# Kernel tuning notes

Hardware: AMD Instinct MI355X
Metric: run time of the kernel (lower is better)

## Reference

```python
import jax, jax.numpy as jnp
import numpy as np

COMMITMENT_WEIGHT = 1.0


def setup_inputs() -> dict:
    key = jax.random.key(0)
    k1, k2 = jax.random.split(key)
    N, D, K, H = 32768, 512, 8192, 1
    x = jax.random.normal(k1, (N, D), dtype=jnp.float32)
    embed = jax.random.normal(k2, (H, K, D), dtype=jnp.float32)
    return {"x": x, "embed": embed}


def reference(x, embed):
    # x: [N, D] -> add codebook dim (needs_codebook_dim path): [H, N, D]
    xf = x.astype(jnp.float32)[None, ...]                      # [1, N, D]
    x_sq = jnp.sum(xf * xf, axis=-1, keepdims=True)            # [H, N, 1]
    e_sq = jnp.sum(embed * embed, axis=-1)                     # [H, K]
    dots = jnp.einsum('hnd,hkd->hnk', xf, embed)               # [H, N, K]
    dist = x_sq - 2.0 * dots + e_sq[:, None, :]                # [H, N, K]
    embed_ind = jnp.argmin(dist, axis=-1)                      # [H, N]
    # codebook lookup (equivalent to one_hot @ embed)
    quantize = jax.vmap(lambda e, i: e[i])(embed, embed_ind)   # [H, N, D]
    # commitment loss (quantize detached vs encoder output)
    commit_loss = jnp.mean((jax.lax.stop_gradient(quantize) - xf) ** 2) * COMMITMENT_WEIGHT
    # straight-through estimator
    quantize = xf + jax.lax.stop_gradient(quantize - xf)
    # drop the added codebook dim
    return quantize[0], embed_ind[0], commit_loss
```

## Files before the change

### kernel.cpp

```cpp
#include <hip/hip_runtime.h>

#define N_ROWS 32768
#define DIM 512
#define K_CODES 8192

#define TMI 128
#define TNI 256
#define BKE 64
#define NKTI (DIM / BKE)
#define QSCALE 32.0f
#define SCL (2.0f / (QSCALE * QSCALE))
#define EPS_I8 5.0f
#define QMARG 2.2f
#define SLOTS 64

#define BN 64
#define BK 256
#define BD 32

typedef __attribute__((ext_vector_type(8))) short bf16x8;
typedef __attribute__((ext_vector_type(4))) float f32x4;
typedef __attribute__((ext_vector_type(4))) int i32x4;

#define AS1 __attribute__((address_space(1)))
#define AS3 __attribute__((address_space(3)))

__device__ inline unsigned int ord_f32(float f) {
    unsigned int u = __float_as_uint(f);
    return (u & 0x80000000u) ? ~u : (u | 0x80000000u);
}
__device__ inline float unord_f32(unsigned int u) {
    unsigned int b = (u & 0x80000000u) ? (u & 0x7fffffffu) : ~u;
    return __uint_as_float(b);
}
__device__ inline int q8(float f) {
    int t = __float2int_rn(f * QSCALE);
    t = t < -127 ? -127 : t;
    t = t > 127 ? 127 : t;
    return t & 255;
}
__device__ inline int pack4(float4 v) {
    return q8(v.x) | (q8(v.y) << 8) | (q8(v.z) << 16) | (q8(v.w) << 24);
}

__global__ __launch_bounds__(256) void esq_kernel(const float* __restrict__ embed,
                                                  float* __restrict__ e_sq) {
    int code = blockIdx.x * 4 + (threadIdx.x >> 6);
    int lane = threadIdx.x & 63;
    const float4* row = (const float4*)(embed + (size_t)code * DIM);
    float s = 0.f;
#pragma unroll
    for (int i = 0; i < 2; ++i) {
        float4 v = row[lane + i * 64];
        s += v.x * v.x + v.y * v.y + v.z * v.z + v.w * v.w;
    }
#pragma unroll
    for (int off = 32; off > 0; off >>= 1) s += __shfl_down(s, off);
    if (lane == 0) e_sq[code] = s;
}

__global__ __launch_bounds__(256) void cvt_embed_i8_kernel(const float* __restrict__ embed,
                                                           signed char* __restrict__ eq,
                                                           float* __restrict__ e_sq) {
    int code = blockIdx.x * 4 + (threadIdx.x >> 6);
    int lane = threadIdx.x & 63;
    const float4* row = (const float4*)(embed + (size_t)code * DIM);
    float4 v0 = row[lane * 2], v1 = row[lane * 2 + 1];
    float s = v0.x * v0.x + v0.y * v0.y + v0.z * v0.z + v0.w * v0.w
            + v1.x * v1.x + v1.y * v1.y + v1.z * v1.z + v1.w * v1.w;
    int2 o;
    o.x = pack4(v0);
    o.y = pack4(v1);
    *(int2*)(eq + (size_t)code * DIM + lane * 8) = o;
#pragma unroll
    for (int off = 32; off > 0; off >>= 1) s += __shfl_down(s, off);
    if (lane == 0) e_sq[code] = s;
}

__global__ __launch_bounds__(256) void cvt_x_i8_kernel(const float* __restrict__ in,
                                                       signed char* __restrict__ out, int n16) {
    int i = blockIdx.x * 256 + threadIdx.x;
    if (i >= n16) return;
    const float4* p = (const float4*)in + (size_t)i * 4;
    float4 v0 = p[0], v1 = p[1], v2 = p[2], v3 = p[3];
    int4 o;
    o.x = pack4(v0); o.y = pack4(v1); o.z = pack4(v2); o.w = pack4(v3);
    ((int4*)out)[i] = o;
}

__global__ __launch_bounds__(512, 4) void passA_i8_kernel(const signed char* __restrict__ xq,
                                                          const signed char* __restrict__ eq,
                                                          const float* __restrict__ e_sq,
                                                          unsigned int* __restrict__ cand_count,
                                                          unsigned int* __restrict__ cands) {
    __shared__ __align__(16) signed char As[3][TMI * BKE];
    __shared__ __align__(16) signed char Bs[3][TNI * BKE];

    const int tid = threadIdx.x;
    const int lane = tid & 63;
    const int wv = tid >> 6;
    const int wm = wv >> 2, wn = wv & 3;
    const int l15 = lane & 15, l4 = lane >> 4;
    const int slot = l4 ^ ((l15 >> 1) & 3);

    const int bid = blockIdx.x;
    const int xcd = bid & 7, idx = bid >> 3;
    const int bx = xcd * 4 + (idx >> 8);
    const int by = idx & 255;
    const int row0 = by * TMI;
    const int col0 = bx * TNI;

    const int cA = tid, cB0 = tid, cB1 = tid + 512;
    const int qA = ((cA & 3) ^ ((cA >> 3) & 3)) * 16;
    const int qB0 = ((cB0 & 3) ^ ((cB0 >> 3) & 3)) * 16;
    const int qB1 = ((cB1 & 3) ^ ((cB1 >> 3) & 3)) * 16;
    const signed char* xr = xq + (size_t)(row0 + (cA >> 2)) * DIM + qA;
    const signed char* er0 = eq + (size_t)(col0 + (cB0 >> 2)) * DIM + qB0;
    const signed char* er1 = eq + (size_t)(col0 + (cB1 >> 2)) * DIM + qB1;

    i32x4 acc[4][4];
#pragma unroll
    for (int m = 0; m < 4; ++m)
#pragma unroll
        for (int n = 0; n < 4; ++n) acc[m][n] = i32x4{0, 0, 0, 0};

#define STAGE(sl, kt)                                                                               \
    do {                                                                                            \
        __builtin_amdgcn_global_load_lds((const AS1 void*)(xr + (kt)),                              \
                                         (AS3 void*)&As[sl][cA * 16], 16, 0, 0);                    \
        __builtin_amdgcn_global_load_lds((const AS1 void*)(er0 + (kt)),                             \
                                         (AS3 void*)&Bs[sl][cB0 * 16], 16, 0, 0);                   \
        __builtin_amdgcn_global_load_lds((const AS1 void*)(er1 + (kt)),                             \
                                         (AS3 void*)&Bs[sl][cB1 * 16], 16, 0, 0);                   \
    } while (0)

    STAGE(0, 0);
    STAGE(1, BKE);
#pragma unroll
    for (int t = 0; t < NKTI; ++t) {
        if (t + 1 < NKTI) {
            asm volatile("s_waitcnt vmcnt(3)" ::: "memory");
        } else {
            asm volatile("s_waitcnt vmcnt(0)" ::: "memory");
        }
        __builtin_amdgcn_s_barrier();
        if (t + 2 < NKTI) STAGE((t + 2) % 3, (t + 2) * BKE);
        const int buf = t % 3;
        i32x4 bfr[4], af[4];
#pragma unroll
        for (int n = 0; n < 4; ++n)
            bfr[n] = *(const i32x4*)&Bs[buf][(wn * 64 + n * 16 + l15) * BKE + slot * 16];
#pragma unroll
        for (int m = 0; m < 4; ++m)
            af[m] = *(const i32x4*)&As[buf][(wm * 64 + m * 16 + l15) * BKE + slot * 16];
        __builtin_amdgcn_s_setprio(1);
#pragma unroll
        for (int m = 0; m < 4; ++m)
#pragma unroll
            for (int n = 0; n < 4; ++n)
                acc[m][n] = __builtin_amdgcn_mfma_i32_16x16x64_i8(af[m], bfr[n], acc[m][n], 0, 0, 0);
        __builtin_amdgcn_s_setprio(0);
    }
#undef STAGE

    unsigned int* row_min = (unsigned int*)&As[0][0];

    float esr[4];
#pragma unroll
    for (int n = 0; n < 4; ++n) esr[n] = e_sq[col0 + wn * 64 + n * 16 + l15];

    __syncthreads();
    if (tid < TMI) row_min[tid] = 0xFFFFFFFFu;
    __syncthreads();
#pragma unroll
    for (int m = 0; m < 4; ++m) {
        float rv[4];
#pragma unroll
        for (int r = 0; r < 4; ++r) rv[r] = 3.4e38f;
#pragma unroll
        for (int n = 0; n < 4; ++n)
#pragma unroll
            for (int r = 0; r < 4; ++r) {
                float s = fmaf(-SCL, (float)acc[m][n][r], esr[n]);
                acc[m][n][r] = __float_as_int(s);
                rv[r] = fminf(rv[r], s);
            }
#pragma unroll
        for (int d = 1; d < 16; d <<= 1)
#pragma unroll
            for (int r = 0; r < 4; ++r) rv[r] = fminf(rv[r], __shfl_xor(rv[r], d));
        if (l15 == 0) {
#pragma unroll
            for (int r = 0; r < 4; ++r)
                atomicMin(&row_min[wm * 64 + m * 16 + l4 * 4 + r], ord_f32(rv[r]));
        }
    }
    __syncthreads();
#pragma unroll
    for (int m = 0; m < 4; ++m)
#pragma unroll
        for (int r = 0; r < 4; ++r) {
            const int lrow = wm * 64 + m * 16 + l4 * 4 + r;
            const float th = unord_f32(row_min[lrow]) + EPS_I8;
            const int grow = row0 + lrow;
#pragma unroll
            for (int n = 0; n < 4; ++n) {
                float sv = __int_as_float(acc[m][n][r]);
                if (sv <= th) {
                    unsigned int s = atomicAdd(&cand_count[grow], 1u);
                    if (s < SLOTS) {
                        unsigned int code = (unsigned)(col0 + wn * 64 + n * 16 + l15);
                        cands[(size_t)grow * SLOTS + s] = (ord_f32(sv) & 0xFFFFE000u) | code;
                    }
                }
            }
        }
}

__global__ __launch_bounds__(256) void passA_fp32_kernel(const float* __restrict__ x,
                                                         const float* __restrict__ embed,
                                                         const float* __restrict__ e_sq,
                                                         unsigned int* __restrict__ cand_count,
                                                         unsigned int* __restrict__ cands,
                                                         int slots) {
    __shared__ float xs[BD][BN];
    __shared__ float es[BD][BK];
    __shared__ float bbest[BN];
    __shared__ unsigned long long smin[BN][33];

    const int tid = threadIdx.x;
    const int tx = tid & 31, ty = tid >> 5;
    const int kb = blockIdx.x * BK;
    const int nb = blockIdx.y * BN;

    float acc[8][8];
#pragma unroll
    for (int i = 0; i < 8; ++i)
#pragma unroll
        for (int j = 0; j < 8; ++j) acc[i][j] = 0.f;

    for (int dt = 0; dt < DIM; dt += BD) {
        {
            int row = tid >> 2, seg = tid & 3;
            const float* xp = x + (size_t)(nb + row) * DIM + dt + seg * 4;
            float4 v0 = *(const float4*)(xp);
            float4 v1 = *(const float4*)(xp + 16);
            xs[seg * 4 + 0][row] = v0.x;  xs[seg * 4 + 1][row] = v0.y;
            xs[seg * 4 + 2][row] = v0.z;  xs[seg * 4 + 3][row] = v0.w;
            xs[seg * 4 + 16][row] = v1.x; xs[seg * 4 + 17][row] = v1.y;
            xs[seg * 4 + 18][row] = v1.z; xs[seg * 4 + 19][row] = v1.w;
        }
        {
            const float* ep = embed + (size_t)(kb + tid) * DIM + dt;
            float4 v[8];
#pragma unroll
            for (int i = 0; i < 8; ++i) v[i] = *(const float4*)(ep + i * 4);
#pragma unroll
            for (int i = 0; i < 8; ++i) {
                es[i * 4 + 0][tid] = v[i].x; es[i * 4 + 1][tid] = v[i].y;
                es[i * 4 + 2][tid] = v[i].z; es[i * 4 + 3][tid] = v[i].w;
            }
        }
        __syncthreads();
#pragma unroll
        for (int d = 0; d < BD; ++d) {
            float a[8], b[8];
            float4 a0 = *(const float4*)&xs[d][ty * 8];
            float4 a1 = *(const float4*)&xs[d][ty * 8 + 4];
            a[0] = a0.x; a[1] = a0.y; a[2] = a0.z; a[3] = a0.w;
            a[4] = a1.x; a[5] = a1.y; a[6] = a1.z; a[7] = a1.w;
#pragma unroll
            for (int j = 0; j < 8; ++j) b[j] = es[d][tx + j * 32];
#pragma unroll
            for (int i = 0; i < 8; ++i)
#pragma unroll
                for (int j = 0; j < 8; ++j) acc[i][j] = fmaf(a[i], b[j], acc[i][j]);
        }
        __syncthreads();
    }

    float esr[8];
#pragma unroll
    for (int j = 0; j < 8; ++j) esr[j] = e_sq[kb + tx + j * 32];
#pragma unroll
    for (int i = 0; i < 8; ++i) {
        float best = 3.4e38f;
#pragma unroll
        for (int j = 0; j < 8; ++j) {
            acc[i][j] = fmaf(-2.f, acc[i][j], esr[j]);
            if (acc[i][j] < best) best = acc[i][j];
        }
        smin[ty * 8 + i][tx] = ((unsigned long long)ord_f32(best) << 32);
    }
    __syncthreads();
    if (tid < BN) {
        unsigned long long m = smin[tid][0];
#pragma unroll 4
        for (int c = 1; c < 32; ++c) {
            unsigned long long v = smin[tid][c];
            if (v < m) m = v;
        }
        bbest[tid] = unord_f32((unsigned int)(m >> 32));
    }
    __syncthreads();
#pragma unroll
    for (int i = 0; i < 8; ++i) {
        int row = ty * 8 + i;
        float thr = bbest[row] + 1.5f;
#pragma unroll
        for (int j = 0; j < 8; ++j) {
            if (acc[i][j] <= thr) {
                unsigned int slot = atomicAdd(&cand_count[nb + row], 1u);
                if (slot < (unsigned)slots)
                    cands[(size_t)(nb + row) * slots + slot] =
                        (ord_f32(acc[i][j]) & 0xFFFFE000u) | (unsigned)(kb + tx + j * 32);
            }
        }
    }
}

__global__ __launch_bounds__(256) void refine_kernel(const float* __restrict__ x,
                                                     const float* __restrict__ embed,
                                                     const unsigned int* __restrict__ cand_count,
                                                     const unsigned int* __restrict__ cands,
                                                     int slots,
                                                     float* __restrict__ out_q,
                                                     float* __restrict__ out_ind,
                                                     double* __restrict__ partials) {
    __shared__ double s_score[64];
    __shared__ unsigned int s_idx[64];
    __shared__ unsigned int s_minkey;
    __shared__ int s_ns;
    __shared__ int s_best;
    __shared__ float s_ls[4];

    const int row = blockIdx.x;
    const int tid = threadIdx.x;
    const int wave = tid >> 6, lane = tid & 63;
    const unsigned int craw = cand_count[row];
    const float4* xp = (const float4*)(x + (size_t)row * DIM);

    if (craw <= (unsigned)slots) {
        int c = (int)craw;
        if (c < 1) c = 1;
        if (tid < 64) {
            unsigned int k = (tid < c) ? cands[(size_t)row * slots + tid] : 0xFFFFFFFFu;
#pragma unroll
            for (int d = 1; d < 64; d <<= 1) {
                unsigned int o = (unsigned int)__shfl_xor((int)k, d);
                if (o < k) k = o;
            }
            if (tid == 0) { s_minkey = k; s_ns = 0; }
        }
        __syncthreads();
        const float th = unord_f32(s_minkey & 0xFFFFE000u) + EPS_I8 + QMARG;
        if (tid < c) {
            unsigned int k = cands[(size_t)row * slots + tid];
            if (unord_f32(k & 0xFFFFE000u) <= th) {
                int sl = atomicAdd(&s_ns, 1);
                s_idx[sl] = k & 0x1FFFu;
            }
        }
        __syncthreads();
        const int ns = s_ns;
        for (int ci = wave; ci < ns; ci += 4) {
            unsigned int k = s_idx[ci];
            const float4* ep = (const float4*)(embed + (size_t)k * DIM);
            double s = 0.0;
#pragma unroll
            for (int i = 0; i < 2; ++i) {
                float4 ev = ep[lane + i * 64];
                float4 xv = xp[lane + i * 64];
                s += (double)ev.x * ((double)ev.x - 2.0 * (double)xv.x);
                s += (double)ev.y * ((double)ev.y - 2.0 * (double)xv.y);
                s += (double)ev.z * ((double)ev.z - 2.0 * (double)xv.z);
                s += (double)ev.w * ((double)ev.w - 2.0 * (double)xv.w);
            }
#pragma unroll
            for (int off = 32; off > 0; off >>= 1) s += __shfl_down(s, off);
            if (lane == 0) s_score[ci] = s;
        }
        __syncthreads();
        if (tid == 0) {
            double best = s_score[0];
            unsigned int bidx = s_idx[0];
            for (int ci = 1; ci < ns; ++ci) {
                double sv = s_score[ci];
                unsigned int k = s_idx[ci];
                if (sv < best || (sv == best && k < bidx)) { best = sv; bidx = k; }
            }
            s_best = (int)bidx;
            out_ind[row] = (float)bidx;
        }
    } else {
        double wbest = 1e300;
        int wbidx = 0;
        for (int k = wave; k < K_CODES; k += 4) {
            const float4* ep = (const float4*)(embed + (size_t)k * DIM);
            double s = 0.0;
#pragma unroll
            for (int i = 0; i < 2; ++i) {
                float4 ev = ep[lane + i * 64];
                float4 xv = xp[lane + i * 64];
                s += (double)ev.x * ((double)ev.x - 2.0 * (double)xv.x);
                s += (double)ev.y * ((double)ev.y - 2.0 * (double)xv.y);
                s += (double)ev.z * ((double)ev.z - 2.0 * (double)xv.z);
                s += (double)ev.w * ((double)ev.w - 2.0 * (double)xv.w);
            }
#pragma unroll
            for (int off = 32; off > 0; off >>= 1) s += __shfl_down(s, off);
            if (lane == 0 && s < wbest) { wbest = s; wbidx = k; }
        }
        if (lane == 0) { s_score[wave] = wbest; s_idx[wave] = (unsigned)wbidx; }
        __syncthreads();
        if (tid == 0) {
            double best = s_score[0];
            unsigned int bidx = s_idx[0];
            for (int w = 1; w < 4; ++w) {
                if (s_score[w] < best || (s_score[w] == best && s_idx[w] < bidx)) {
                    best = s_score[w]; bidx = s_idx[w];
                }
            }
            s_best = (int)bidx;
            out_ind[row] = (float)bidx;
        }
    }
    __syncthreads();
    const int k = s_best;
    const float2* x2 = (const float2*)(x + (size_t)row * DIM);
    const float2* e2 = (const float2*)(embed + (size_t)k * DIM);
    float2* o2 = (float2*)(out_q + (size_t)row * DIM);
    float2 xv = x2[tid], ev = e2[tid];
    float2 o;
    o.x = xv.x + (ev.x - xv.x);
    o.y = xv.y + (ev.y - xv.y);
    o2[tid] = o;
    float dx = ev.x - xv.x, dy = ev.y - xv.y;
    float ls = dx * dx + dy * dy;
#pragma unroll
    for (int off = 32; off > 0; off >>= 1) ls += __shfl_down(ls, off);
    if (lane == 0) s_ls[wave] = ls;
    __syncthreads();
    if (tid == 0) partials[row] = (double)(s_ls[0] + s_ls[1] + s_ls[2] + s_ls[3]);
}

__global__ __launch_bounds__(1024) void finalize_kernel(const double* __restrict__ partials,
                                                        float* __restrict__ out_loss) {
    __shared__ double sm[1024];
    double s = 0.0;
    for (int i = threadIdx.x; i < N_ROWS; i += 1024) s += partials[i];
    sm[threadIdx.x] = s;
    __syncthreads();
    for (int off = 512; off > 0; off >>= 1) {
        if (threadIdx.x < off) sm[threadIdx.x] += sm[threadIdx.x + off];
        __syncthreads();
    }
    if (threadIdx.x == 0) *out_loss = (float)(sm[0] / ((double)N_ROWS * (double)DIM));
}

extern "C" void kernel_launch(void* const* d_in, const int* in_sizes, int n_in,
                              void* d_out, int out_size, void* d_ws, size_t ws_size,
                              hipStream_t stream) {
    const float* x = (const float*)d_in[0];
    const float* embed = (const float*)d_in[1];
    float* out = (float*)d_out;
    float* out_q = out;
    float* out_ind = out + (size_t)N_ROWS * DIM;
    float* out_loss = out_ind + N_ROWS;

    char* ws = (char*)d_ws;
    float* e_sq = (float*)(ws + 16);
    unsigned int* counts = (unsigned int*)(ws + 16 + 32768);
    double* partials = (double*)(ws + 16 + 32768 + 131072);
    char* dyn = ws + 16 + 32768 + 131072 + 262144;
    size_t fixed = (size_t)16 + 32768 + 131072 + 262144;
    size_t dyn_avail = ws_size > fixed ? ws_size - fixed : 0;

    const size_t xq_b = (size_t)N_ROWS * DIM;
    const size_t eq_b = (size_t)K_CODES * DIM;
    const size_t need_i8 = xq_b + eq_b + (size_t)N_ROWS * SLOTS * 4;

    hipMemsetAsync(counts, 0, (size_t)N_ROWS * 4, stream);

    if (dyn_avail >= need_i8) {
        signed char* xq = (signed char*)dyn;
        signed char* eq = (signed char*)(dyn + xq_b);
        unsigned int* cands = (unsigned int*)(dyn + xq_b + eq_b);
        cvt_embed_i8_kernel<<<K_CODES / 4, 256, 0, stream>>>(embed, eq, e_sq);
        cvt_x_i8_kernel<<<(N_ROWS * DIM / 16 + 255) / 256, 256, 0, stream>>>(x, xq, N_ROWS * DIM / 16);
        passA_i8_kernel<<<(K_CODES / TNI) * (N_ROWS / TMI), 512, 0, stream>>>(xq, eq, e_sq, counts, cands);
        refine_kernel<<<N_ROWS, 256, 0, stream>>>(x, embed, counts, cands, SLOTS, out_q, out_ind, partials);
    } else {
        esq_kernel<<<K_CODES / 4, 256, 0, stream>>>(embed, e_sq);
        unsigned int* cands = (unsigned int*)dyn;
        int slots = 40;
        size_t avail = dyn_avail / ((size_t)N_ROWS * 4);
        if (avail < (size_t)slots) slots = (int)avail;
        if (slots < 2) slots = 2;
        passA_fp32_kernel<<<dim3(K_CODES / BK, N_ROWS / BN), 256, 0, stream>>>(x, embed, e_sq, counts, cands, slots);
        refine_kernel<<<N_ROWS, 256, 0, stream>>>(x, embed, counts, cands, slots, out_q, out_ind, partials);
    }
    finalize_kernel<<<1, 1024, 0, stream>>>(partials, out_loss);
}
```

Baseline: 476.3 us.

## Enlarge int8 distance GEMM tile to 256x256 with double-buffered LDS

Doubles the row tile of the int8 distance pass so each wave computes 128x64 outputs, raising arithmetic intensity and halving reloads of codebook tiles. LDS staging changes from a three-deep to a two-deep ring, with an explicit barrier after each k-step to protect the buffer being overwritten. The trade-off is much higher accumulator register pressure under the same launch bounds, fewer blocks in the grid, and less latency hiding from the shallower pipeline.

```diff
diff --git a/kernel.cpp b/kernel.cpp
--- a/kernel.cpp
+++ b/kernel.cpp
@@ -4,7 +4,7 @@
 #define DIM 512
 #define K_CODES 8192
 
-#define TMI 128
+#define TMI 256
 #define TNI 256
 #define BKE 64
 #define NKTI (DIM / BKE)
@@ -18,7 +18,6 @@
 #define BK 256
 #define BD 32
 
-typedef __attribute__((ext_vector_type(8))) short bf16x8;
 typedef __attribute__((ext_vector_type(4))) float f32x4;
 typedef __attribute__((ext_vector_type(4))) int i32x4;
 
@@ -93,8 +92,8 @@
                                                           const float* __restrict__ e_sq,
                                                           unsigned int* __restrict__ cand_count,
                                                           unsigned int* __restrict__ cands) {
-    __shared__ __align__(16) signed char As[3][TMI * BKE];
-    __shared__ __align__(16) signed char Bs[3][TNI * BKE];
+    __shared__ __align__(16) signed char As[2][TMI * BKE];
+    __shared__ __align__(16) signed char Bs[2][TNI * BKE];
 
     const int tid = threadIdx.x;
     const int lane = tid & 63;
@@ -105,61 +104,66 @@
 
     const int bid = blockIdx.x;
     const int xcd = bid & 7, idx = bid >> 3;
-    const int bx = xcd * 4 + (idx >> 8);
-    const int by = idx & 255;
+    const int bx = xcd * 4 + (idx >> 7);
+    const int by = idx & 127;
     const int row0 = by * TMI;
     const int col0 = bx * TNI;
 
-    const int cA = tid, cB0 = tid, cB1 = tid + 512;
-    const int qA = ((cA & 3) ^ ((cA >> 3) & 3)) * 16;
-    const int qB0 = ((cB0 & 3) ^ ((cB0 >> 3) & 3)) * 16;
-    const int qB1 = ((cB1 & 3) ^ ((cB1 >> 3) & 3)) * 16;
-    const signed char* xr = xq + (size_t)(row0 + (cA >> 2)) * DIM + qA;
-    const signed char* er0 = eq + (size_t)(col0 + (cB0 >> 2)) * DIM + qB0;
-    const signed char* er1 = eq + (size_t)(col0 + (cB1 >> 2)) * DIM + qB1;
-
-    i32x4 acc[4][4];
-#pragma unroll
-    for (int m = 0; m < 4; ++m)
+    const int c0 = tid, c1 = tid + 512;
+    const int q0 = ((c0 & 3) ^ ((c0 >> 3) & 3)) * 16;
+    const int q1 = ((c1 & 3) ^ ((c1 >> 3) & 3)) * 16;
+    const signed char* xr0 = xq + (size_t)(row0 + (c0 >> 2)) * DIM + q0;
+    const signed char* xr1 = xq + (size_t)(row0 + (c1 >> 2)) * DIM + q1;
+    const signed char* er0 = eq + (size_t)(col0 + (c0 >> 2)) * DIM + q0;
+    const signed char* er1 = eq + (size_t)(col0 + (c1 >> 2)) * DIM + q1;
+
+    i32x4 acc[8][4];
+#pragma unroll
+    for (int m = 0; m < 8; ++m)
 #pragma unroll
         for (int n = 0; n < 4; ++n) acc[m][n] = i32x4{0, 0, 0, 0};
 
 #define STAGE(sl, kt)                                                                               \
     do {                                                                                            \
-        __builtin_amdgcn_global_load_lds((const AS1 void*)(xr + (kt)),                              \
-                                         (AS3 void*)&As[sl][cA * 16], 16, 0, 0);                    \
+        __builtin_amdgcn_global_load_lds((const AS1 void*)(xr0 + (kt)),                             \
+                                         (AS3 void*)&As[sl][c0 * 16], 16, 0, 0);                    \
+        __builtin_amdgcn_global_load_lds((const AS1 void*)(xr1 + (kt)),                             \
+                                         (AS3 void*)&As[sl][c1 * 16], 16, 0, 0);                    \
         __builtin_amdgcn_global_load_lds((const AS1 void*)(er0 + (kt)),                             \
-                                         (AS3 void*)&Bs[sl][cB0 * 16], 16, 0, 0);                   \
+                                         (AS3 void*)&Bs[sl][c0 * 16], 16, 0, 0);                    \
         __builtin_amdgcn_global_load_lds((const AS1 void*)(er1 + (kt)),                             \
-                                         (AS3 void*)&Bs[sl][cB1 * 16], 16, 0, 0);                   \
+                                         (AS3 void*)&Bs[sl][c1 * 16], 16, 0, 0);                    \
     } while (0)
 
     STAGE(0, 0);
-    STAGE(1, BKE);
+    int buf = 0;
 #pragma unroll
     for (int t = 0; t < NKTI; ++t) {
         if (t + 1 < NKTI) {
-            asm volatile("s_waitcnt vmcnt(3)" ::: "memory");
+            STAGE(buf ^ 1, (t + 1) * BKE);
+            asm volatile("s_waitcnt vmcnt(4)" ::: "memory");
         } else {
             asm volatile("s_waitcnt vmcnt(0)" ::: "memory");
         }
         __builtin_amdgcn_s_barrier();
-        if (t + 2 < NKTI) STAGE((t + 2) % 3, (t + 2) * BKE);
-        const int buf = t % 3;
-        i32x4 bfr[4], af[4];
+        i32x4 bfr[4], af[8];
 #pragma unroll
         for (int n = 0; n < 4; ++n)
             bfr[n] = *(const i32x4*)&Bs[buf][(wn * 64 + n * 16 + l15) * BKE + slot * 16];
 #pragma unroll
-        for (int m = 0; m < 4; ++m)
-            af[m] = *(const i32x4*)&As[buf][(wm * 64 + m * 16 + l15) * BKE + slot * 16];
+        for (int m = 0; m < 8; ++m)
+            af[m] = *(const i32x4*)&As[buf][(wm * 128 + m * 16 + l15) * BKE + slot * 16];
         __builtin_amdgcn_s_setprio(1);
 #pragma unroll
-        for (int m = 0; m < 4; ++m)
+        for (int m = 0; m < 8; ++m)
 #pragma unroll
             for (int n = 0; n < 4; ++n)
                 acc[m][n] = __builtin_amdgcn_mfma_i32_16x16x64_i8(af[m], bfr[n], acc[m][n], 0, 0, 0);
         __builtin_amdgcn_s_setprio(0);
+        asm volatile("s_waitcnt lgkmcnt(0)" ::: "memory");
+        __builtin_amdgcn_sched_barrier(0);
+        __builtin_amdgcn_s_barrier();
+        buf ^= 1;
     }
 #undef STAGE
 
@@ -169,11 +173,10 @@
 #pragma unroll
     for (int n = 0; n < 4; ++n) esr[n] = e_sq[col0 + wn * 64 + n * 16 + l15];
 
-    __syncthreads();
     if (tid < TMI) row_min[tid] = 0xFFFFFFFFu;
     __syncthreads();
 #pragma unroll
-    for (int m = 0; m < 4; ++m) {
+    for (int m = 0; m < 8; ++m) {
         float rv[4];
 #pragma unroll
         for (int r = 0; r < 4; ++r) rv[r] = 3.4e38f;
@@ -192,15 +195,15 @@
         if (l15 == 0) {
 #pragma unroll
             for (int r = 0; r < 4; ++r)
-                atomicMin(&row_min[wm * 64 + m * 16 + l4 * 4 + r], ord_f32(rv[r]));
-        }
-    }
-    __syncthreads();
-#pragma unroll
-    for (int m = 0; m < 4; ++m)
+                atomicMin(&row_min[wm * 128 + m * 16 + l4 * 4 + r], ord_f32(rv[r]));
+        }
+    }
+    __syncthreads();
+#pragma unroll
+    for (int m = 0; m < 8; ++m)
 #pragma unroll
         for (int r = 0; r < 4; ++r) {
-            const int lrow = wm * 64 + m * 16 + l4 * 4 + r;
+            const int lrow = wm * 128 + m * 16 + l4 * 4 + r;
             const float th = unord_f32(row_min[lrow]) + EPS_I8;
             const int grow = row0 + lrow;
 #pragma unroll
```

Result: slower. 1.628 ms (+241.9%).
